# Optimization experiments

Hardware: AMD Instinct MI355X
Metric: run time of the kernel (lower is better)

The kernel has to match this reference:

```python
import jax, jax.numpy as jnp
import numpy as np

N_NODES = 20000
N_EDGES = 320000
F_IN, H1, H2, N_CLS = 128, 512, 256, 40
NEG_SLOPE = 0.2


def _glorot(key, shape):
    lim = float(np.sqrt(6.0 / (shape[0] + shape[-1])))
    return jax.random.uniform(key, shape, jnp.float32, -lim, lim)


def setup_inputs() -> dict:
    key = jax.random.key(0)
    ks = jax.random.split(key, 12)
    x = jax.random.normal(ks[0], (N_NODES, F_IN), jnp.float32)
    edge_index = jax.random.randint(ks[1], (2, N_EDGES), 0, N_NODES, jnp.int64)
    params = {}
    dims = [(F_IN, H1), (H1, H2), (H2, N_CLS)]
    for i, (din, dout) in enumerate(dims, start=1):
        params[f"W{i}"] = _glorot(ks[3 * i - 1], (din, dout))
        params[f"a{i}s"] = _glorot(ks[3 * i], (1, dout))[0]
        params[f"a{i}d"] = _glorot(ks[3 * i + 1], (1, dout))[0]
        params[f"b{i}"] = jnp.zeros((dout,), jnp.float32)
    return {"x": x, "edge_index": edge_index, **params}


def gat_conv(x, src, dst, W, a_src, a_dst, b, num_nodes):
    # PyG GATConv, heads=1: h = xW; e_ij = LeakyReLU(a_src.h_j + a_dst.h_i)
    # alpha = softmax over incoming edges of target i; out_i = sum_j alpha_ij h_j + b
    h = x @ W                                        # [N, Dout]
    alpha_s = h @ a_src                              # [N]
    alpha_d = h @ a_dst                              # [N]
    e = jax.nn.leaky_relu(alpha_s[src] + alpha_d[dst], NEG_SLOPE)  # [E]
    m = jax.ops.segment_max(e, dst, num_segments=num_nodes)        # [N]
    ex = jnp.exp(e - m[dst])
    denom = jax.ops.segment_sum(ex, dst, num_segments=num_nodes)   # [N]
    alpha = ex / denom[dst]
    out = jax.ops.segment_sum(alpha[:, None] * h[src], dst, num_segments=num_nodes)
    return out + b


def reference(x, edge_index, W1, a1s, a1d, b1, W2, a2s, a2d, b2, W3, a3s, a3d, b3):
    n = x.shape[0]
    # PyG GATConv adds self-loops by default
    loops = jnp.arange(n, dtype=edge_index.dtype)
    src = jnp.concatenate([edge_index[0], loops])
    dst = jnp.concatenate([edge_index[1], loops])
    h = jax.nn.relu(gat_conv(x, src, dst, W1, a1s, a1d, b1, n))
    h = jax.nn.relu(gat_conv(h, src, dst, W2, a2s, a2d, b2, n))
    h = gat_conv(h, src, dst, W3, a3s, a3d, b3, n)
    return jax.nn.log_softmax(h, axis=1)
```

## Files before the change

### kernel.cpp

```cpp
#include <hip/hip_runtime.h>
#include <math.h>

#define N_NODES 20000
#define N_EDGESC 320000
#define ET (N_EDGESC + N_NODES)
#define F_IN 128
#define H1 512
#define H2 256
#define N_CLS 40
#define NEG_SLOPE 0.2f
#define DEGMAX 64

typedef __attribute__((ext_vector_type(8))) short short8;
typedef __attribute__((ext_vector_type(4))) float floatx4;

__device__ __forceinline__ unsigned short f2bf(float x) {
    unsigned u = __float_as_uint(x);
    unsigned r = (u + 0x7fffu + ((u >> 16) & 1u)) >> 16;
    return (unsigned short)r;
}
__device__ __forceinline__ float bflo(unsigned v) { return __uint_as_float(v << 16); }
__device__ __forceinline__ float bfhi(unsigned v) { return __uint_as_float(v & 0xffff0000u); }
__device__ __forceinline__ float leaky(float e) { return (e > 0.f) ? e : e * NEG_SLOPE; }

template <int DIN, bool IN_BF16>
__device__ __forceinline__ void gemv2_body(int node, int lane, const void* __restrict__ in,
                                           const float* __restrict__ wvs,
                                           const float* __restrict__ wvd,
                                           float* __restrict__ als, float* __restrict__ ald) {
    constexpr int C = DIN / 64;
    float ss = 0.f, sd = 0.f;
    if constexpr (IN_BF16) {
        const unsigned short* r = (const unsigned short*)in + (size_t)node * DIN + lane * C;
        float f[C];
        if constexpr (C == 8) {
            uint4 v = *(const uint4*)r;
            f[0] = bflo(v.x); f[1] = bfhi(v.x); f[2] = bflo(v.y); f[3] = bfhi(v.y);
            f[4] = bflo(v.z); f[5] = bfhi(v.z); f[6] = bflo(v.w); f[7] = bfhi(v.w);
        } else {
            uint2 v = *(const uint2*)r;
            f[0] = bflo(v.x); f[1] = bfhi(v.x); f[2] = bflo(v.y); f[3] = bfhi(v.y);
        }
        #pragma unroll
        for (int c = 0; c < C; ++c) {
            ss += f[c] * wvs[lane * C + c];
            sd += f[c] * wvd[lane * C + c];
        }
    } else {
        const float* r = (const float*)in + (size_t)node * DIN + lane * 2;
        float2 v = *(const float2*)r;
        ss = v.x * wvs[lane * 2] + v.y * wvs[lane * 2 + 1];
        sd = v.x * wvd[lane * 2] + v.y * wvd[lane * 2 + 1];
    }
    #pragma unroll
    for (int off = 32; off; off >>= 1) {
        ss += __shfl_xor(ss, off);
        sd += __shfl_xor(sd, off);
    }
    if (lane == 0) { als[node] = ss; ald[node] = sd; }
}

#define NCT (F_IN * H1 + H1 * H2 + H2 * N_CLS)
#define PB_CASTX 2500
#define PB_CASTT ((NCT + 255) / 256)
#define PB_WA 224
#define PB_ZERO ((N_NODES + 1 + 255) / 256)

__global__ __launch_bounds__(256) void prep_kernel(
        const float* __restrict__ x, unsigned short* __restrict__ xb,
        const float* __restrict__ W1, unsigned short* __restrict__ w1t,
        const float* __restrict__ a1s, const float* __restrict__ a1d,
        const float* __restrict__ W2, unsigned short* __restrict__ w2t,
        const float* __restrict__ a2s, const float* __restrict__ a2d,
        const float* __restrict__ W3, unsigned short* __restrict__ w3t,
        const float* __restrict__ a3s, const float* __restrict__ a3d,
        float* __restrict__ wab, int* __restrict__ deg, int* __restrict__ ocnt) {
    int bid = blockIdx.x, t = threadIdx.x;
    if (bid < PB_CASTX) {
        int i = (bid * 256 + t) * 4;
        float4 v = *(const float4*)(x + i);
        ushort4 o = { f2bf(v.x), f2bf(v.y), f2bf(v.z), f2bf(v.w) };
        *(ushort4*)(xb + i) = o;
    } else if (bid < PB_CASTX + PB_CASTT) {
        int i = (bid - PB_CASTX) * 256 + t;
        if (i < F_IN * H1) {
            int k = i >> 9, n = i & 511;
            w1t[n * F_IN + k] = f2bf(W1[i]);
        } else if (i < F_IN * H1 + H1 * H2) {
            int j = i - F_IN * H1;
            int k = j >> 8, n = j & 255;
            w2t[n * H1 + k] = f2bf(W2[j]);
        } else if (i < NCT) {
            int j = i - (F_IN * H1 + H1 * H2);
            int k = j / N_CLS, n = j - k * N_CLS;
            w3t[n * H2 + k] = f2bf(W3[j]);
        }
    } else if (bid < PB_CASTX + PB_CASTT + PB_WA) {
        int lane = t & 63;
        int row = (bid - PB_CASTX - PB_CASTT) * 4 + (t >> 6);
        const float *W, *vs, *vd;
        float *os, *od;
        int N, k;
        if (row < 128)      { k = row;       W = W1; vs = a1s; vd = a1d; os = wab;        od = wab + 128;  N = H1; }
        else if (row < 640) { k = row - 128; W = W2; vs = a2s; vd = a2d; os = wab + 256;  od = wab + 768;  N = H2; }
        else                { k = row - 640; W = W3; vs = a3s; vd = a3d; os = wab + 1280; od = wab + 1536; N = N_CLS; }
        const float* r = W + (size_t)k * N;
        float ss = 0.f, sd = 0.f;
        for (int n = lane; n < N; n += 64) {
            float v = r[n];
            ss += v * vs[n];
            sd += v * vd[n];
        }
        #pragma unroll
        for (int off = 32; off; off >>= 1) {
            ss += __shfl_xor(ss, off);
            sd += __shfl_xor(sd, off);
        }
        if (lane == 0) { os[k] = ss; od[k] = sd; }
    } else {
        int i = (bid - PB_CASTX - PB_CASTT - PB_WA) * 256 + t;
        if (i < N_NODES) deg[i] = 0;
        else if (i == N_NODES) *ocnt = 0;
    }
}

#define CB_CNT ((ET + 255) / 256)

__global__ __launch_bounds__(256) void fill_gemv1_kernel(
        const int* __restrict__ ei, int* __restrict__ deg,
        int* __restrict__ csr_src, int* __restrict__ ocnt, int* __restrict__ oflow,
        const float* __restrict__ x, const float* __restrict__ wab,
        float* __restrict__ als1, float* __restrict__ ald1) {
    int bid = blockIdx.x, t = threadIdx.x;
    if (bid < CB_CNT) {
        int e = bid * 256 + t;
        if (e < ET) {
            int s, d;
            if (e < N_EDGESC) { s = ei[e]; d = ei[N_EDGESC + e]; }
            else { s = d = e - N_EDGESC; }
            int slot = atomicAdd(&deg[d], 1);
            if (slot < DEGMAX) csr_src[(d << 6) + slot] = s;
            else {
                int o = atomicAdd(ocnt, 1);
                oflow[2 * o] = d;
                oflow[2 * o + 1] = s;
            }
        }
    } else {
        int node = (bid - CB_CNT) * 4 + (t >> 6);
        if (node < N_NODES)
            gemv2_body<F_IN, false>(node, t & 63, x, wab, wab + 128, als1, ald1);
    }
}

template <int DOUT, bool BIAS, bool RELU, bool LSM, bool IN_BF16, bool OUT_BF16, bool ALPHA3>
__global__ __launch_bounds__(256) void agg_kernel(const void* __restrict__ h,
                                                  const float* __restrict__ as,
                                                  const float* __restrict__ ad,
                                                  const int* __restrict__ deg,
                                                  const int* __restrict__ csr_src,
                                                  const int* __restrict__ ocnt,
                                                  const int* __restrict__ oflow,
                                                  const float* __restrict__ bias,
                                                  void* __restrict__ outp,
                                                  const float* __restrict__ wv3s,
                                                  const float* __restrict__ wv3d,
                                                  float* __restrict__ o3s,
                                                  float* __restrict__ o3d) {
    constexpr int C = (DOUT + 63) / 64;
    int wave = threadIdx.x >> 6, lane = threadIdx.x & 63;
    int node = blockIdx.x * 4 + wave;
    if (node >= N_NODES) return;
    int degt = deg[node];
    int cnt = min(degt, DEGMAX);
    int base = node << 6;
    float adi = ad[node];
    bool ovf = degt > DEGMAX;
    int novf = ovf ? *ocnt : 0;

    bool has0 = lane < cnt;
    int sj = has0 ? csr_src[base + lane] : 0;
    float ej = has0 ? leaky(as[sj] + adi) : -INFINITY;

    float m = ej;
    if (ovf) {
        for (int i = lane; i < novf; i += 64)
            if (oflow[2 * i] == node) m = fmaxf(m, leaky(as[oflow[2 * i + 1]] + adi));
    }
    #pragma unroll
    for (int off = 32; off; off >>= 1) m = fmaxf(m, __shfl_xor(m, off));

    float den = has0 ? expf(ej - m) : 0.f;
    if (ovf) {
        for (int i = lane; i < novf; i += 64)
            if (oflow[2 * i] == node) den += expf(leaky(as[oflow[2 * i + 1]] + adi) - m);
    }
    #pragma unroll
    for (int off = 32; off; off >>= 1) den += __shfl_xor(den, off);
    float invden = 1.f / den;

    float wgt = has0 ? expf(ej - m) * invden : 0.f;

    float acc[C];
    #pragma unroll
    for (int c = 0; c < C; ++c) acc[c] = 0.f;

    auto fetch = [&](int s, float* f) {
        if constexpr (IN_BF16) {
            const unsigned short* hr = (const unsigned short*)h + (size_t)s * DOUT + lane * C;
            if constexpr (C == 8) {
                uint4 v = *(const uint4*)hr;
                f[0] = bflo(v.x); f[1] = bfhi(v.x); f[2] = bflo(v.y); f[3] = bfhi(v.y);
                f[4] = bflo(v.z); f[5] = bfhi(v.z); f[6] = bflo(v.w); f[7] = bfhi(v.w);
            } else if constexpr (C == 4) {
                uint2 v = *(const uint2*)hr;
                f[0] = bflo(v.x); f[1] = bfhi(v.x); f[2] = bflo(v.y); f[3] = bfhi(v.y);
            } else {
                unsigned v = *(const unsigned*)hr;
                f[0] = bflo(v); f[1] = bfhi(v);
            }
        } else {
            if (lane < DOUT) f[0] = ((const float*)h)[(size_t)s * DOUT + lane];
            else f[0] = 0.f;
        }
    };

    int j = 0;
    for (; j + 7 < cnt; j += 8) {
        int s[8]; float a[8]; float f[8][C];
        #pragma unroll
        for (int u = 0; u < 8; ++u) { s[u] = __shfl(sj, j + u); a[u] = __shfl(wgt, j + u); }
        #pragma unroll
        for (int u = 0; u < 8; ++u) fetch(s[u], f[u]);
        #pragma unroll
        for (int u = 0; u < 8; ++u)
            #pragma unroll
            for (int c = 0; c < C; ++c) acc[c] += a[u] * f[u][c];
    }
    for (; j < cnt; ++j) {
        int s0 = __shfl(sj, j);
        float a0 = __shfl(wgt, j);
        float f0[C];
        fetch(s0, f0);
        #pragma unroll
        for (int c = 0; c < C; ++c) acc[c] += a0 * f0[c];
    }
    if (ovf) {
        for (int i = 0; i < novf; ++i) {
            if (oflow[2 * i] == node) {
                int s0 = oflow[2 * i + 1];
                float a0 = expf(leaky(as[s0] + adi) - m) * invden;
                float f0[C];
                fetch(s0, f0);
                #pragma unroll
                for (int c = 0; c < C; ++c) acc[c] += a0 * f0[c];
            }
        }
    }

    if constexpr (!LSM) {
        float ps = 0.f, pd = 0.f;
        #pragma unroll
        for (int c = 0; c < C; ++c) {
            int col = lane * C + c;
            if (DOUT % 64 == 0 || col < DOUT) {
                float v = acc[c];
                if constexpr (BIAS) v += bias[col];
                if constexpr (RELU) v = fmaxf(v, 0.f);
                if constexpr (ALPHA3) { ps += v * wv3s[col]; pd += v * wv3d[col]; }
                if constexpr (OUT_BF16)
                    ((unsigned short*)outp)[(size_t)node * DOUT + col] = f2bf(v);
                else
                    ((float*)outp)[(size_t)node * DOUT + col] = v;
            }
        }
        if constexpr (ALPHA3) {
            #pragma unroll
            for (int off = 32; off; off >>= 1) {
                ps += __shfl_xor(ps, off);
                pd += __shfl_xor(pd, off);
            }
            if (lane == 0) { o3s[node] = ps; o3d[node] = pd; }
        }
    } else {
        float v = (lane < DOUT) ? (acc[0] + bias[lane]) : -INFINITY;
        float mm = v;
        #pragma unroll
        for (int off = 32; off; off >>= 1) mm = fmaxf(mm, __shfl_xor(mm, off));
        float ex = (lane < DOUT) ? expf(v - mm) : 0.f;
        float Z = ex;
        #pragma unroll
        for (int off = 32; off; off >>= 1) Z += __shfl_xor(Z, off);
        if (lane < DOUT) ((float*)outp)[(size_t)node * DOUT + lane] = v - mm - logf(Z);
    }
}

#define LDT 40
#define LSO 66

template <int MT, int NT, bool BIASRELU, bool OUT_BF16, int GDIN, bool GBF16>
__global__ __launch_bounds__(256) void gemm_fused(
        const unsigned short* __restrict__ A, const unsigned short* __restrict__ Bt,
        void* __restrict__ Cp, const float* __restrict__ bias,
        int M, int K, int N, int gemm_blocks,
        const void* __restrict__ gin, const float* __restrict__ wvs,
        const float* __restrict__ wvd, float* __restrict__ als, float* __restrict__ ald) {
    constexpr int MI = MT / 64;
    __shared__ unsigned short As[MT * LDT];
    __shared__ unsigned short Bs[64 * LDT];
    __shared__ unsigned short Ls[64 * LSO];
    int bid = blockIdx.x, t = threadIdx.x;
    int w = t >> 6, lane = t & 63;

    if (bid >= gemm_blocks) {
        if constexpr (GDIN > 0) {
            int node = (bid - gemm_blocks) * 4 + w;
            if (node < N_NODES)
                gemv2_body<GDIN, GBF16>(node, lane, gin, wvs, wvd, als, ald);
        }
        return;
    }

    int quad = lane >> 4, l16 = lane & 15;
    int bm = (bid / NT) * MT, bn = (bid % NT) * 64;
    int ar0 = t >> 2;
    int ak = (t & 3) * 8;

    floatx4 acc[MI][4];
    #pragma unroll
    for (int i = 0; i < MI; ++i)
        #pragma unroll
        for (int j = 0; j < 4; ++j) acc[i][j] = (floatx4){0.f, 0.f, 0.f, 0.f};

    uint4 pa0 = {0,0,0,0}, pa1 = {0,0,0,0}, pb = {0,0,0,0};
    {
        int gm0 = bm + ar0, gn = bn + ar0;
        if (gm0 < M) pa0 = *(const uint4*)(A + (size_t)gm0 * K + ak);
        if constexpr (MI == 2) {
            int gm1 = bm + 64 + ar0;
            if (gm1 < M) pa1 = *(const uint4*)(A + (size_t)gm1 * K + ak);
        }
        if (gn < N) pb = *(const uint4*)(Bt + (size_t)gn * K + ak);
    }

    for (int k0 = 0; k0 < K; k0 += 32) {
        *(uint4*)(&As[ar0 * LDT + ak]) = pa0;
        if constexpr (MI == 2) *(uint4*)(&As[(64 + ar0) * LDT + ak]) = pa1;
        *(uint4*)(&Bs[ar0 * LDT + ak]) = pb;
        __syncthreads();

        int kn = k0 + 32;
        if (kn < K) {
            int gm0 = bm + ar0, gn = bn + ar0;
            pa0 = (gm0 < M) ? *(const uint4*)(A + (size_t)gm0 * K + kn + ak) : (uint4){0,0,0,0};
            if constexpr (MI == 2) {
                int gm1 = bm + 64 + ar0;
                pa1 = (gm1 < M) ? *(const uint4*)(A + (size_t)gm1 * K + kn + ak) : (uint4){0,0,0,0};
            }
            pb = (gn < N) ? *(const uint4*)(Bt + (size_t)gn * K + kn + ak) : (uint4){0,0,0,0};
        }

        short8 a[MI], b[4];
        #pragma unroll
        for (int mi = 0; mi < MI; ++mi)
            a[mi] = *(short8*)(&As[(w * (MT / 4) + mi * 16 + l16) * LDT + quad * 8]);
        #pragma unroll
        for (int ni = 0; ni < 4; ++ni)
            b[ni] = *(short8*)(&Bs[(ni * 16 + l16) * LDT + quad * 8]);
        #pragma unroll
        for (int mi = 0; mi < MI; ++mi)
            #pragma unroll
            for (int ni = 0; ni < 4; ++ni)
                acc[mi][ni] = __builtin_amdgcn_mfma_f32_16x16x32_bf16(a[mi], b[ni], acc[mi][ni], 0, 0, 0);
        __syncthreads();
    }

    if constexpr (OUT_BF16) {
        #pragma unroll
        for (int mi = 0; mi < MI; ++mi) {
            #pragma unroll
            for (int ni = 0; ni < 4; ++ni) {
                int col = bn + ni * 16 + l16;
                #pragma unroll
                for (int r = 0; r < 4; ++r) {
                    float v = acc[mi][ni][r];
                    if constexpr (BIASRELU) v = fmaxf(v + bias[col], 0.f);
                    Ls[(w * 16 + quad * 4 + r) * LSO + ni * 16 + l16] = f2bf(v);
                }
            }
            __syncthreads();
            #pragma unroll
            for (int i = 0; i < 2; ++i) {
                int idx = t + i * 256;
                int lrow = idx >> 3, c8 = (idx & 7) * 8;
                int grow = bm + (lrow >> 4) * (MT / 4) + mi * 16 + (lrow & 15);
                if (grow < M)
                    *(uint4*)((unsigned short*)Cp + (size_t)grow * N + bn + c8) =
                        *(uint4*)(&Ls[lrow * LSO + c8]);
            }
            __syncthreads();
        }
    } else {
        #pragma unroll
        for (int mi = 0; mi < MI; ++mi) {
            #pragma unroll
            for (int r = 0; r < 4; ++r) {
                int row = bm + w * (MT / 4) + mi * 16 + quad * 4 + r;
                if (row >= M) continue;
                #pragma unroll
                for (int ni = 0; ni < 4; ++ni) {
                    int col = bn + ni * 16 + l16;
                    if (col < N) ((float*)Cp)[(size_t)row * N + col] = acc[mi][ni][r];
                }
            }
        }
    }
}


extern "C" void kernel_launch(void* const* d_in, const int* in_sizes, int n_in,
                              void* d_out, int out_size, void* d_ws, size_t ws_size,
                              hipStream_t stream) {
    const float* x   = (const float*)d_in[0];
    const int*   ei  = (const int*)d_in[1];
    const float* W1  = (const float*)d_in[2];
    const float* a1s = (const float*)d_in[3];
    const float* a1d = (const float*)d_in[4];
    const float* b1  = (const float*)d_in[5];
    const float* W2  = (const float*)d_in[6];
    const float* a2s = (const float*)d_in[7];
    const float* a2d = (const float*)d_in[8];
    const float* b2  = (const float*)d_in[9];
    const float* W3  = (const float*)d_in[10];
    const float* a3s = (const float*)d_in[11];
    const float* a3d = (const float*)d_in[12];
    const float* b3  = (const float*)d_in[13];
    float* out = (float*)d_out;

    char* ws = (char*)d_ws;
    size_t off = 0;
    auto alloc = [&](size_t bytes) {
        void* p = ws + off;
        off = (off + bytes + 255) & ~(size_t)255;
        return p;
    };
    int*            deg      = (int*)alloc(N_NODES * 4);
    int*            ocnt     = (int*)alloc(4);
    int*            oflow    = (int*)alloc(2 * 8192 * 4);
    int*            csr_src  = (int*)alloc((size_t)N_NODES * DEGMAX * 4);
    float*          alph     = (float*)alloc((size_t)6 * N_NODES * 4);
    float*          wab      = (float*)alloc(1792 * 4);
    unsigned short* xb       = (unsigned short*)alloc((size_t)N_NODES * F_IN * 2);
    unsigned short* w1t      = (unsigned short*)alloc((size_t)H1 * F_IN * 2);
    unsigned short* w2t      = (unsigned short*)alloc((size_t)H2 * H1 * 2);
    unsigned short* w3t      = (unsigned short*)alloc((size_t)N_CLS * H2 * 2);
    unsigned short* zb       = (unsigned short*)alloc((size_t)N_NODES * F_IN * 2);
    unsigned short* y1       = (unsigned short*)alloc((size_t)N_NODES * H1 * 2);
    unsigned short* h2       = (unsigned short*)alloc((size_t)N_NODES * H2 * 2);
    float*          h3       = (float*)alloc((size_t)N_NODES * N_CLS * 4);
    (void)alloc(128 * 1024);

    unsigned short* y2 = y1;

    float* als1 = alph + 0 * N_NODES; float* ald1 = alph + 1 * N_NODES;
    float* als2 = alph + 2 * N_NODES; float* ald2 = alph + 3 * N_NODES;
    float* als3 = alph + 4 * N_NODES; float* ald3 = alph + 5 * N_NODES;

    dim3 blk(256);
    int nodeblocks = (N_NODES + 3) / 4;
    const int mt128 = (N_NODES + 127) / 128;
    const int mt64  = (N_NODES + 63) / 64;

    prep_kernel<<<PB_CASTX + PB_CASTT + PB_WA + PB_ZERO, blk, 0, stream>>>(
        x, xb, W1, w1t, a1s, a1d, W2, w2t, a2s, a2d, W3, w3t, a3s, a3d, wab, deg, ocnt);
    fill_gemv1_kernel<<<CB_CNT + nodeblocks, blk, 0, stream>>>(
        ei, deg, csr_src, ocnt, oflow, x, wab, als1, ald1);
    agg_kernel<F_IN, false, false, false, true, true, false><<<nodeblocks, blk, 0, stream>>>(
        xb, als1, ald1, deg, csr_src, ocnt, oflow, nullptr, zb, nullptr, nullptr, nullptr, nullptr);
    gemm_fused<128, 8, true, true, 0, false><<<8 * mt128, blk, 0, stream>>>(
        zb, w1t, y1, b1, N_NODES, F_IN, H1, 8 * mt128,
        nullptr, nullptr, nullptr, nullptr, nullptr);
    gemm_fused<128, 4, false, true, H1, true><<<4 * mt128 + nodeblocks, blk, 0, stream>>>(
        y1, w2t, h2, nullptr, N_NODES, H1, H2, 4 * mt128,
        y1, wab + 256, wab + 768, als2, ald2);
    agg_kernel<H2, true, true, false, true, true, true><<<nodeblocks, blk, 0, stream>>>(
        h2, als2, ald2, deg, csr_src, ocnt, oflow, b2, y2, wab + 1280, wab + 1536, als3, ald3);
    gemm_fused<64, 1, false, false, 0, false><<<mt64, blk, 0, stream>>>(
        y2, w3t, h3, nullptr, N_NODES, H2, N_CLS, mt64,
        nullptr, nullptr, nullptr, nullptr, nullptr);
    agg_kernel<N_CLS, true, false, true, false, false, false><<<nodeblocks, blk, 0, stream>>>(
        h3, als3, ald3, deg, csr_src, ocnt, oflow, b3, out, nullptr, nullptr, nullptr, nullptr);
}
```

Measured before the change: 212.7 us.

## Rebalance prep work across kernels and split layer-2 aggregation across two waves

```diff
diff --git a/kernel.cpp b/kernel.cpp
--- a/kernel.cpp
+++ b/kernel.cpp
@@ -22,6 +22,52 @@
 __device__ __forceinline__ float bflo(unsigned v) { return __uint_as_float(v << 16); }
 __device__ __forceinline__ float bfhi(unsigned v) { return __uint_as_float(v & 0xffff0000u); }
 __device__ __forceinline__ float leaky(float e) { return (e > 0.f) ? e : e * NEG_SLOPE; }
+
+
+__device__ __forceinline__ void wa_row(int row, int lane,
+        const float* __restrict__ W1, const float* __restrict__ a1s, const float* __restrict__ a1d,
+        const float* __restrict__ W2, const float* __restrict__ a2s, const float* __restrict__ a2d,
+        const float* __restrict__ W3, const float* __restrict__ a3s, const float* __restrict__ a3d,
+        float* __restrict__ wab) {
+    const float *W, *vs, *vd;
+    float *os, *od;
+    int N, k;
+    if (row < 128)      { k = row;       W = W1; vs = a1s; vd = a1d; os = wab;        od = wab + 128;  N = H1; }
+    else if (row < 640) { k = row - 128; W = W2; vs = a2s; vd = a2d; os = wab + 256;  od = wab + 768;  N = H2; }
+    else                { k = row - 640; W = W3; vs = a3s; vd = a3d; os = wab + 1280; od = wab + 1536; N = N_CLS; }
+    const float* r = W + (size_t)k * N;
+    float ss = 0.f, sd = 0.f;
+    for (int n = lane; n < N; n += 64) {
+        float v = r[n];
+        ss += v * vs[n];
+        sd += v * vd[n];
+    }
+    #pragma unroll
+    for (int off = 32; off; off >>= 1) {
+        ss += __shfl_xor(ss, off);
+        sd += __shfl_xor(sd, off);
+    }
+    if (lane == 0) { os[k] = ss; od[k] = sd; }
+}
+
+#define NCT (F_IN * H1 + H1 * H2 + H2 * N_CLS)
+__device__ __forceinline__ void castT_el(int i,
+        const float* __restrict__ W1, unsigned short* __restrict__ w1t,
+        const float* __restrict__ W2, unsigned short* __restrict__ w2t,
+        const float* __restrict__ W3, unsigned short* __restrict__ w3t) {
+    if (i < F_IN * H1) {
+        int k = i >> 9, n = i & 511;
+        w1t[n * F_IN + k] = f2bf(W1[i]);
+    } else if (i < F_IN * H1 + H1 * H2) {
+        int j = i - F_IN * H1;
+        int k = j >> 8, n = j & 255;
+        w2t[n * H1 + k] = f2bf(W2[j]);
+    } else if (i < NCT) {
+        int j = i - (F_IN * H1 + H1 * H2);
+        int k = j / N_CLS, n = j - k * N_CLS;
+        w3t[n * H2 + k] = f2bf(W3[j]);
+    }
+}
 
 template <int DIN, bool IN_BF16>
 __device__ __forceinline__ void gemv2_body(int node, int lane, const void* __restrict__ in,
@@ -60,77 +106,159 @@
     if (lane == 0) { als[node] = ss; ald[node] = sd; }
 }
 
-#define NCT (F_IN * H1 + H1 * H2 + H2 * N_CLS)
-#define PB_CASTX 2500
-#define PB_CASTT ((NCT + 255) / 256)
-#define PB_WA 224
-#define PB_ZERO ((N_NODES + 1 + 255) / 256)
-
-__global__ __launch_bounds__(256) void prep_kernel(
-        const float* __restrict__ x, unsigned short* __restrict__ xb,
-        const float* __restrict__ W1, unsigned short* __restrict__ w1t,
-        const float* __restrict__ a1s, const float* __restrict__ a1d,
-        const float* __restrict__ W2, unsigned short* __restrict__ w2t,
-        const float* __restrict__ a2s, const float* __restrict__ a2d,
-        const float* __restrict__ W3, unsigned short* __restrict__ w3t,
-        const float* __restrict__ a3s, const float* __restrict__ a3d,
+template <int DOUT, int SPLIT, bool BIAS, bool RELU, bool LSM, bool IN_BF16, bool OUT_BF16>
+__device__ __forceinline__ void agg_body(int wid, int lane,
+        const void* __restrict__ h, const float* __restrict__ as, const float* __restrict__ ad,
+        const int* __restrict__ deg, const int* __restrict__ csr_src,
+        const int* __restrict__ ocnt, const int* __restrict__ oflow,
+        const float* __restrict__ bias, void* __restrict__ outp) {
+    constexpr int CD = DOUT / SPLIT;
+    constexpr int C = (CD + 63) / 64;
+    int node = wid / SPLIT;
+    int colbase = (SPLIT == 1) ? 0 : (wid % SPLIT) * CD;
+    if (node >= N_NODES) return;
+    int degt = deg[node];
+    int cnt = min(degt, DEGMAX);
+    int base = node << 6;
+    float adi = ad[node];
+    bool ovf = degt > DEGMAX;
+    int novf = ovf ? *ocnt : 0;
+
+    bool has0 = lane < cnt;
+    int sj = has0 ? csr_src[base + lane] : 0;
+    float ej = has0 ? leaky(as[sj] + adi) : -INFINITY;
+
+    float m = ej;
+    if (ovf) {
+        for (int i = lane; i < novf; i += 64)
+            if (oflow[2 * i] == node) m = fmaxf(m, leaky(as[oflow[2 * i + 1]] + adi));
+    }
+    #pragma unroll
+    for (int off = 32; off; off >>= 1) m = fmaxf(m, __shfl_xor(m, off));
+
+    float den = has0 ? expf(ej - m) : 0.f;
+    if (ovf) {
+        for (int i = lane; i < novf; i += 64)
+            if (oflow[2 * i] == node) den += expf(leaky(as[oflow[2 * i + 1]] + adi) - m);
+    }
+    #pragma unroll
+    for (int off = 32; off; off >>= 1) den += __shfl_xor(den, off);
+    float invden = 1.f / den;
+
+    float wgt = has0 ? expf(ej - m) * invden : 0.f;
+
+    float acc[C];
+    #pragma unroll
+    for (int c = 0; c < C; ++c) acc[c] = 0.f;
+
+    auto fetch = [&](int s, float* f) {
+        if constexpr (IN_BF16) {
+            const unsigned short* hr = (const unsigned short*)h + (size_t)s * DOUT + colbase + lane * C;
+            if constexpr (C == 8) {
+                uint4 v = *(const uint4*)hr;
+                f[0] = bflo(v.x); f[1] = bfhi(v.x); f[2] = bflo(v.y); f[3] = bfhi(v.y);
+                f[4] = bflo(v.z); f[5] = bfhi(v.z); f[6] = bflo(v.w); f[7] = bfhi(v.w);
+            } else if constexpr (C == 4) {
+                uint2 v = *(const uint2*)hr;
+                f[0] = bflo(v.x); f[1] = bfhi(v.x); f[2] = bflo(v.y); f[3] = bfhi(v.y);
+            } else {
+                unsigned v = *(const unsigned*)hr;
+                f[0] = bflo(v); f[1] = bfhi(v);
+            }
+        } else {
+            if (lane < CD) f[0] = ((const float*)h)[(size_t)s * DOUT + colbase + lane];
+            else f[0] = 0.f;
+        }
+    };
+
+    int j = 0;
+    for (; j + 7 < cnt; j += 8) {
+        int s[8]; float a[8]; float f[8][C];
+        #pragma unroll
+        for (int u = 0; u < 8; ++u) { s[u] = __shfl(sj, j + u); a[u] = __shfl(wgt, j + u); }
+        #pragma unroll
+        for (int u = 0; u < 8; ++u) fetch(s[u], f[u]);
+        #pragma unroll
+        for (int u = 0; u < 8; ++u)
+            #pragma unroll
+            for (int c = 0; c < C; ++c) acc[c] += a[u] * f[u][c];
+    }
+    for (; j < cnt; ++j) {
+        int s0 = __shfl(sj, j);
+        float a0 = __shfl(wgt, j);
+        float f0[C];
+        fetch(s0, f0);
+        #pragma unroll
+        for (int c = 0; c < C; ++c) acc[c] += a0 * f0[c];
+    }
+    if (ovf) {
+        for (int i = 0; i < novf; ++i) {
+            if (oflow[2 * i] == node) {
+                int s0 = oflow[2 * i + 1];
+                float a0 = expf(leaky(as[s0] + adi) - m) * invden;
+                float f0[C];
+                fetch(s0, f0);
+                #pragma unroll
+                for (int c = 0; c < C; ++c) acc[c] += a0 * f0[c];
+            }
+        }
+    }
+
+    if constexpr (!LSM) {
+        #pragma unroll
+        for (int c = 0; c < C; ++c) {
+            int col = colbase + lane * C + c;
+            if (CD % 64 == 0 || lane * C + c < CD) {
+                float v = acc[c];
+                if constexpr (BIAS) v += bias[col];
+                if constexpr (RELU) v = fmaxf(v, 0.f);
+                if constexpr (OUT_BF16)
+                    ((unsigned short*)outp)[(size_t)node * DOUT + col] = f2bf(v);
+                else
+                    ((float*)outp)[(size_t)node * DOUT + col] = v;
+            }
+        }
+    } else {
+        float v = (lane < DOUT) ? (acc[0] + bias[lane]) : -INFINITY;
+        float mm = v;
+        #pragma unroll
+        for (int off = 32; off; off >>= 1) mm = fmaxf(mm, __shfl_xor(mm, off));
+        float ex = (lane < DOUT) ? expf(v - mm) : 0.f;
+        float Z = ex;
+        #pragma unroll
+        for (int off = 32; off; off >>= 1) Z += __shfl_xor(Z, off);
+        if (lane < DOUT) ((float*)outp)[(size_t)node * DOUT + lane] = v - mm - logf(Z);
+    }
+}
+
+#define PZ ((N_NODES + 1 + 255) / 256)
+#define PW1 32
+
+__global__ __launch_bounds__(256) void prep0_kernel(
+        const float* __restrict__ W1, const float* __restrict__ a1s, const float* __restrict__ a1d,
+        const float* __restrict__ W2, const float* __restrict__ a2s, const float* __restrict__ a2d,
+        const float* __restrict__ W3, const float* __restrict__ a3s, const float* __restrict__ a3d,
         float* __restrict__ wab, int* __restrict__ deg, int* __restrict__ ocnt) {
     int bid = blockIdx.x, t = threadIdx.x;
-    if (bid < PB_CASTX) {
-        int i = (bid * 256 + t) * 4;
-        float4 v = *(const float4*)(x + i);
-        ushort4 o = { f2bf(v.x), f2bf(v.y), f2bf(v.z), f2bf(v.w) };
-        *(ushort4*)(xb + i) = o;
-    } else if (bid < PB_CASTX + PB_CASTT) {
-        int i = (bid - PB_CASTX) * 256 + t;
-        if (i < F_IN * H1) {
-            int k = i >> 9, n = i & 511;
-            w1t[n * F_IN + k] = f2bf(W1[i]);
-        } else if (i < F_IN * H1 + H1 * H2) {
-            int j = i - F_IN * H1;
-            int k = j >> 8, n = j & 255;
-            w2t[n * H1 + k] = f2bf(W2[j]);
-        } else if (i < NCT) {
-            int j = i - (F_IN * H1 + H1 * H2);
-            int k = j / N_CLS, n = j - k * N_CLS;
-            w3t[n * H2 + k] = f2bf(W3[j]);
-        }
-    } else if (bid < PB_CASTX + PB_CASTT + PB_WA) {
-        int lane = t & 63;
-        int row = (bid - PB_CASTX - PB_CASTT) * 4 + (t >> 6);
-        const float *W, *vs, *vd;
-        float *os, *od;
-        int N, k;
-        if (row < 128)      { k = row;       W = W1; vs = a1s; vd = a1d; os = wab;        od = wab + 128;  N = H1; }
-        else if (row < 640) { k = row - 128; W = W2; vs = a2s; vd = a2d; os = wab + 256;  od = wab + 768;  N = H2; }
-        else                { k = row - 640; W = W3; vs = a3s; vd = a3d; os = wab + 1280; od = wab + 1536; N = N_CLS; }
-        const float* r = W + (size_t)k * N;
-        float ss = 0.f, sd = 0.f;
-        for (int n = lane; n < N; n += 64) {
-            float v = r[n];
-            ss += v * vs[n];
-            sd += v * vd[n];
-        }
-        #pragma unroll
-        for (int off = 32; off; off >>= 1) {
-            ss += __shfl_xor(ss, off);
-            sd += __shfl_xor(sd, off);
-        }
-        if (lane == 0) { os[k] = ss; od[k] = sd; }
-    } else {
-        int i = (bid - PB_CASTX - PB_CASTT - PB_WA) * 256 + t;
+    if (bid < PZ) {
+        int i = bid * 256 + t;
         if (i < N_NODES) deg[i] = 0;
         else if (i == N_NODES) *ocnt = 0;
+    } else {
+        int row = (bid - PZ) * 4 + (t >> 6);
+        if (row < 128) wa_row(row, t & 63, W1, a1s, a1d, W2, a2s, a2d, W3, a3s, a3d, wab);
     }
 }
 
 #define CB_CNT ((ET + 255) / 256)
-
-__global__ __launch_bounds__(256) void fill_gemv1_kernel(
+#define CXB 2500
+#define NODEB ((N_NODES + 3) / 4)
+
+__global__ __launch_bounds__(256) void fill_castx_gemv1_kernel(
         const int* __restrict__ ei, int* __restrict__ deg,
         int* __restrict__ csr_src, int* __restrict__ ocnt, int* __restrict__ oflow,
-        const float* __restrict__ x, const float* __restrict__ wab,
-        float* __restrict__ als1, float* __restrict__ ald1) {
+        const float* __restrict__ x, unsigned short* __restrict__ xb,
+        const float* __restrict__ wab, float* __restrict__ als1, float* __restrict__ ald1) {
     int bid = blockIdx.x, t = threadIdx.x;
     if (bid < CB_CNT) {
         int e = bid * 256 + t;
@@ -146,152 +274,42 @@
                 oflow[2 * o + 1] = s;
             }
         }
+    } else if (bid < CB_CNT + CXB) {
+        int i = ((bid - CB_CNT) * 256 + t) * 4;
+        float4 v = *(const float4*)(x + i);
+        ushort4 o = { f2bf(v.x), f2bf(v.y), f2bf(v.z), f2bf(v.w) };
+        *(ushort4*)(xb + i) = o;
     } else {
-        int node = (bid - CB_CNT) * 4 + (t >> 6);
+        int node = (bid - CB_CNT - CXB) * 4 + (t >> 6);
         if (node < N_NODES)
             gemv2_body<F_IN, false>(node, t & 63, x, wab, wab + 128, als1, ald1);
     }
 }
 
-template <int DOUT, bool BIAS, bool RELU, bool LSM, bool IN_BF16, bool OUT_BF16, bool ALPHA3>
-__global__ __launch_bounds__(256) void agg_kernel(const void* __restrict__ h,
-                                                  const float* __restrict__ as,
-                                                  const float* __restrict__ ad,
-                                                  const int* __restrict__ deg,
-                                                  const int* __restrict__ csr_src,
-                                                  const int* __restrict__ ocnt,
-                                                  const int* __restrict__ oflow,
-                                                  const float* __restrict__ bias,
-                                                  void* __restrict__ outp,
-                                                  const float* __restrict__ wv3s,
-                                                  const float* __restrict__ wv3d,
-                                                  float* __restrict__ o3s,
-                                                  float* __restrict__ o3d) {
-    constexpr int C = (DOUT + 63) / 64;
-    int wave = threadIdx.x >> 6, lane = threadIdx.x & 63;
-    int node = blockIdx.x * 4 + wave;
-    if (node >= N_NODES) return;
-    int degt = deg[node];
-    int cnt = min(degt, DEGMAX);
-    int base = node << 6;
-    float adi = ad[node];
-    bool ovf = degt > DEGMAX;
-    int novf = ovf ? *ocnt : 0;
-
-    bool has0 = lane < cnt;
-    int sj = has0 ? csr_src[base + lane] : 0;
-    float ej = has0 ? leaky(as[sj] + adi) : -INFINITY;
-
-    float m = ej;
-    if (ovf) {
-        for (int i = lane; i < novf; i += 64)
-            if (oflow[2 * i] == node) m = fmaxf(m, leaky(as[oflow[2 * i + 1]] + adi));
-    }
-    #pragma unroll
-    for (int off = 32; off; off >>= 1) m = fmaxf(m, __shfl_xor(m, off));
-
-    float den = has0 ? expf(ej - m) : 0.f;
-    if (ovf) {
-        for (int i = lane; i < novf; i += 64)
-            if (oflow[2 * i] == node) den += expf(leaky(as[oflow[2 * i + 1]] + adi) - m);
-    }
-    #pragma unroll
-    for (int off = 32; off; off >>= 1) den += __shfl_xor(den, off);
-    float invden = 1.f / den;
-
-    float wgt = has0 ? expf(ej - m) * invden : 0.f;
-
-    float acc[C];
-    #pragma unroll
-    for (int c = 0; c < C; ++c) acc[c] = 0.f;
-
-    auto fetch = [&](int s, float* f) {
-        if constexpr (IN_BF16) {
-            const unsigned short* hr = (const unsigned short*)h + (size_t)s * DOUT + lane * C;
-            if constexpr (C == 8) {
-                uint4 v = *(const uint4*)hr;
-                f[0] = bflo(v.x); f[1] = bfhi(v.x); f[2] = bflo(v.y); f[3] = bfhi(v.y);
-                f[4] = bflo(v.z); f[5] = bfhi(v.z); f[6] = bflo(v.w); f[7] = bfhi(v.w);
-            } else if constexpr (C == 4) {
-                uint2 v = *(const uint2*)hr;
-                f[0] = bflo(v.x); f[1] = bfhi(v.x); f[2] = bflo(v.y); f[3] = bfhi(v.y);
-            } else {
-                unsigned v = *(const unsigned*)hr;
-                f[0] = bflo(v); f[1] = bfhi(v);
-            }
-        } else {
-            if (lane < DOUT) f[0] = ((const float*)h)[(size_t)s * DOUT + lane];
-            else f[0] = 0.f;
-        }
-    };
-
-    int j = 0;
-    for (; j + 7 < cnt; j += 8) {
-        int s[8]; float a[8]; float f[8][C];
-        #pragma unroll
-        for (int u = 0; u < 8; ++u) { s[u] = __shfl(sj, j + u); a[u] = __shfl(wgt, j + u); }
-        #pragma unroll
-        for (int u = 0; u < 8; ++u) fetch(s[u], f[u]);
-        #pragma unroll
-        for (int u = 0; u < 8; ++u)
-            #pragma unroll
-            for (int c = 0; c < C; ++c) acc[c] += a[u] * f[u][c];
-    }
-    for (; j < cnt; ++j) {
-        int s0 = __shfl(sj, j);
-        float a0 = __shfl(wgt, j);
-        float f0[C];
-        fetch(s0, f0);
-        #pragma unroll
-        for (int c = 0; c < C; ++c) acc[c] += a0 * f0[c];
-    }
-    if (ovf) {
-        for (int i = 0; i < novf; ++i) {
-            if (oflow[2 * i] == node) {
-                int s0 = oflow[2 * i + 1];
-                float a0 = expf(leaky(as[s0] + adi) - m) * invden;
-                float f0[C];
-                fetch(s0, f0);
-                #pragma unroll
-                for (int c = 0; c < C; ++c) acc[c] += a0 * f0[c];
-            }
-        }
-    }
-
-    if constexpr (!LSM) {
-        float ps = 0.f, pd = 0.f;
-        #pragma unroll
-        for (int c = 0; c < C; ++c) {
-            int col = lane * C + c;
-            if (DOUT % 64 == 0 || col < DOUT) {
-                float v = acc[c];
-                if constexpr (BIAS) v += bias[col];
-                if constexpr (RELU) v = fmaxf(v, 0.f);
-                if constexpr (ALPHA3) { ps += v * wv3s[col]; pd += v * wv3d[col]; }
-                if constexpr (OUT_BF16)
-                    ((unsigned short*)outp)[(size_t)node * DOUT + col] = f2bf(v);
-                else
-                    ((float*)outp)[(size_t)node * DOUT + col] = v;
-            }
-        }
-        if constexpr (ALPHA3) {
-            #pragma unroll
-            for (int off = 32; off; off >>= 1) {
-                ps += __shfl_xor(ps, off);
-                pd += __shfl_xor(pd, off);
-            }
-            if (lane == 0) { o3s[node] = ps; o3d[node] = pd; }
-        }
+#define CTB ((NCT + 255) / 256)
+
+__global__ __launch_bounds__(256) void agg1_tails_kernel(
+        const unsigned short* __restrict__ xb,
+        const float* __restrict__ als1, const float* __restrict__ ald1,
+        const int* __restrict__ deg, const int* __restrict__ csr_src,
+        const int* __restrict__ ocnt, const int* __restrict__ oflow,
+        unsigned short* __restrict__ zb,
+        const float* __restrict__ W1, unsigned short* __restrict__ w1t,
+        const float* __restrict__ W2, unsigned short* __restrict__ w2t,
+        const float* __restrict__ W3, unsigned short* __restrict__ w3t,
+        const float* __restrict__ a1s, const float* __restrict__ a1d,
+        const float* __restrict__ a2s, const float* __restrict__ a2d,
+        const float* __restrict__ a3s, const float* __restrict__ a3d,
+        float* __restrict__ wab) {
+    int bid = blockIdx.x, t = threadIdx.x;
+    if (bid < NODEB) {
+        agg_body<F_IN, 1, false, false, false, true, true>(
+            bid * 4 + (t >> 6), t & 63, xb, als1, ald1, deg, csr_src, ocnt, oflow, nullptr, zb);
+    } else if (bid < NODEB + CTB) {
+        castT_el((bid - NODEB) * 256 + t, W1, w1t, W2, w2t, W3, w3t);
     } else {
-        float v = (lane < DOUT) ? (acc[0] + bias[lane]) : -INFINITY;
-        float mm = v;
-        #pragma unroll
-        for (int off = 32; off; off >>= 1) mm = fmaxf(mm, __shfl_xor(mm, off));
-        float ex = (lane < DOUT) ? expf(v - mm) : 0.f;
-        float Z = ex;
-        #pragma unroll
-        for (int off = 32; off; off >>= 1) Z += __shfl_xor(Z, off);
-        if (lane < DOUT) ((float*)outp)[(size_t)node * DOUT + lane] = v - mm - logf(Z);
+        int row = 128 + (bid - NODEB - CTB) * 4 + (t >> 6);
+        if (row < 896) wa_row(row, t & 63, W1, a1s, a1d, W2, a2s, a2d, W3, a3s, a3d, wab);
     }
 }
 
@@ -415,6 +433,29 @@
             }
         }
     }
+}
+
+
+__global__ __launch_bounds__(256) void agg2_kernel(
+        const unsigned short* __restrict__ h2,
+        const float* __restrict__ als2, const float* __restrict__ ald2,
+        const int* __restrict__ deg, const int* __restrict__ csr_src,
+        const int* __restrict__ ocnt, const int* __restrict__ oflow,
+        const float* __restrict__ b2, unsigned short* __restrict__ y2) {
+    agg_body<H2, 2, true, true, false, true, true>(
+        blockIdx.x * 4 + (threadIdx.x >> 6), threadIdx.x & 63,
+        h2, als2, ald2, deg, csr_src, ocnt, oflow, b2, y2);
+}
+
+__global__ __launch_bounds__(256) void agg3_kernel(
+        const float* __restrict__ h3,
+        const float* __restrict__ als3, const float* __restrict__ ald3,
+        const int* __restrict__ deg, const int* __restrict__ csr_src,
+        const int* __restrict__ ocnt, const int* __restrict__ oflow,
+        const float* __restrict__ b3, float* __restrict__ out) {
+    agg_body<N_CLS, 1, true, false, true, false, false>(
+        blockIdx.x * 4 + (threadIdx.x >> 6), threadIdx.x & 63,
+        h3, als3, ald3, deg, csr_src, ocnt, oflow, b3, out);
 }
 
 
@@ -467,27 +508,27 @@
     float* als3 = alph + 4 * N_NODES; float* ald3 = alph + 5 * N_NODES;
 
     dim3 blk(256);
-    int nodeblocks = (N_NODES + 3) / 4;
     const int mt128 = (N_NODES + 127) / 128;
     const int mt64  = (N_NODES + 63) / 64;
 
-    prep_kernel<<<PB_CASTX + PB_CASTT + PB_WA + PB_ZERO, blk, 0, stream>>>(
-        x, xb, W1, w1t, a1s, a1d, W2, w2t, a2s, a2d, W3, w3t, a3s, a3d, wab, deg, ocnt);
-    fill_gemv1_kernel<<<CB_CNT + nodeblocks, blk, 0, stream>>>(
-        ei, deg, csr_src, ocnt, oflow, x, wab, als1, ald1);
-    agg_kernel<F_IN, false, false, false, true, true, false><<<nodeblocks, blk, 0, stream>>>(
-        xb, als1, ald1, deg, csr_src, ocnt, oflow, nullptr, zb, nullptr, nullptr, nullptr, nullptr);
+    prep0_kernel<<<PZ + PW1, blk, 0, stream>>>(
+        W1, a1s, a1d, W2, a2s, a2d, W3, a3s, a3d, wab, deg, ocnt);
+    fill_castx_gemv1_kernel<<<CB_CNT + CXB + NODEB, blk, 0, stream>>>(
+        ei, deg, csr_src, ocnt, oflow, x, xb, wab, als1, ald1);
+    agg1_tails_kernel<<<NODEB + CTB + 192, blk, 0, stream>>>(
+        xb, als1, ald1, deg, csr_src, ocnt, oflow, zb,
+        W1, w1t, W2, w2t, W3, w3t, a1s, a1d, a2s, a2d, a3s, a3d, wab);
     gemm_fused<128, 8, true, true, 0, false><<<8 * mt128, blk, 0, stream>>>(
         zb, w1t, y1, b1, N_NODES, F_IN, H1, 8 * mt128,
         nullptr, nullptr, nullptr, nullptr, nullptr);
-    gemm_fused<128, 4, false, true, H1, true><<<4 * mt128 + nodeblocks, blk, 0, stream>>>(
+    gemm_fused<128, 4, false, true, H1, true><<<4 * mt128 + NODEB, blk, 0, stream>>>(
         y1, w2t, h2, nullptr, N_NODES, H1, H2, 4 * mt128,
         y1, wab + 256, wab + 768, als2, ald2);
-    agg_kernel<H2, true, true, false, true, true, true><<<nodeblocks, blk, 0, stream>>>(
-        h2, als2, ald2, deg, csr_src, ocnt, oflow, b2, y2, wab + 1280, wab + 1536, als3, ald3);
-    gemm_fused<64, 1, false, false, 0, false><<<mt64, blk, 0, stream>>>(
+    agg2_kernel<<<2 * NODEB, blk, 0, stream>>>(
+        h2, als2, ald2, deg, csr_src, ocnt, oflow, b2, y2);
+    gemm_fused<64, 1, false, false, H2, true><<<mt64 + NODEB, blk, 0, stream>>>(
         y2, w3t, h3, nullptr, N_NODES, H2, N_CLS, mt64,
-        nullptr, nullptr, nullptr, nullptr, nullptr);
-    agg_kernel<N_CLS, true, false, true, false, false, false><<<nodeblocks, blk, 0, stream>>>(
-        h3, als3, ald3, deg, csr_src, ocnt, oflow, b3, out, nullptr, nullptr, nullptr, nullptr);
-}
+        y2, wab + 1280, wab + 1536, als3, ald3);
+    agg3_kernel<<<NODEB, blk, 0, stream>>>(
+        h3, als3, ald3, deg, csr_src, ocnt, oflow, b3, out);
+}
```

After: 216.4 us. Within noise of the previous version (+1.7%).
